# Optimization experiments

Hardware: AMD Instinct MI355X
Metric: run time of the kernel (lower is better)

## Reference

```python
import jax, jax.numpy as jnp
import numpy as np

B = 4096
ED = 128          # EMBEDDING_DIM
HD = 64           # HIDDEN_DIM
LH = 128          # LSTM_HIDDEN_DIM
IN_DIM = ED * (12 + 48 + 1)  # 7808
N_ABILITY, N_MOVE = 300, 900


def setup_inputs() -> dict:
    key = jax.random.key(0)
    ks = jax.random.split(key, 16)
    s = lambda k, shape, scale=0.05: (jax.random.normal(k, shape, dtype=jnp.float32) * scale)
    return {
        "ability_ids": jax.random.randint(ks[0], (B, 12), 0, N_ABILITY),
        "move_ids": jax.random.randint(ks[1], (B, 48), 0, N_MOVE),
        "numerical": s(ks[2], (B, 84), 1.0),
        "mask": (jax.random.uniform(ks[3], (B, 9)) > 0.3).astype(jnp.float32),
        "h0": jnp.zeros((B, LH), jnp.float32),
        "c0": jnp.zeros((B, LH), jnp.float32),
        "ability_emb": s(ks[4], (N_ABILITY, ED), 1.0),
        "move_emb": s(ks[5], (N_MOVE, ED), 1.0),
        "num_W": s(ks[6], (ED, 84)),
        "num_b": s(ks[7], (ED,)),
        "Wih": s(ks[8], (4 * LH, IN_DIM), 0.01),
        "Whh": s(ks[9], (4 * LH, LH)),
        "bih": s(ks[10], (4 * LH,)),
        "bhh": s(ks[11], (4 * LH,)),
        "W1": s(ks[12], (HD, LH)),
        "b1": s(ks[13], (HD,)),
        "W2": s(ks[14], (ED, HD)),
        "b2": s(ks[15], (ED,)),
        "Wa": s(jax.random.fold_in(key, 100), (9, ED)),
        "ba": s(jax.random.fold_in(key, 101), (9,)),
    }


def reference(ability_ids, move_ids, numerical, mask, h0, c0,
              ability_emb, move_emb, num_W, num_b,
              Wih, Whh, bih, bhh, W1, b1, W2, b2, Wa, ba):
    # Gather + concat: [B, 12*ED] + [B, 48*ED] + [B, ED] -> [B, 7808]
    ab = ability_emb[ability_ids].reshape(ability_ids.shape[0], 12 * ED)
    mv = move_emb[move_ids].reshape(move_ids.shape[0], 48 * ED)
    num = numerical @ num_W.T + num_b
    x = jnp.concatenate([ab, mv, num], axis=-1)

    # Single-timestep LSTM (torch gate order: i, f, g, o)
    gates = x @ Wih.T + bih + h0 @ Whh.T + bhh
    i, f, g, o = jnp.split(gates, 4, axis=-1)
    i, f, o = jax.nn.sigmoid(i), jax.nn.sigmoid(f), jax.nn.sigmoid(o)
    g = jnp.tanh(g)
    c1 = f * c0 + i * g
    h1 = o * jnp.tanh(c1)

    # MLP head + action logits
    feat = jax.nn.relu(h1 @ W1.T + b1) @ W2.T + b2
    probs = jax.nn.softmax(feat @ Wa.T + ba, axis=-1)

    # Masked renormalization; fall back to unmasked probs when mask kills everything
    masked = probs * mask
    ssum = masked.sum(-1, keepdims=True)
    out = jnp.where(ssum > 0, masked / jnp.where(ssum > 0, ssum, 1.0), probs)
    return out, h1, c1
```

## Files before the change

kernel.cpp:

```cpp
#include <hip/hip_runtime.h>
#include <hip/hip_bf16.h>
#include <stdint.h>
#include <stddef.h>

typedef __bf16 bf16;
typedef __bf16 bf16x8 __attribute__((ext_vector_type(8)));
typedef float f32x4 __attribute__((ext_vector_type(4)));

#define BATCH 4096
#define KIH 7808
#define KTOT 7936
#define NG 512
#define LH 128
#define HD 64
#define ED 128
#define SPLITK 4

#define OFF_WCAT 0u
#define OFF_GPART 8126464u
#define OFF_XT   41680896u
#define OFF_AB   43778048u
#define OFF_MV   43854848u
#define OFF_ADDR 44085248u
#define OFF_H1B  46182400u
#define OFF_W1F  47230976u
#define OFF_W2F  47247360u
#define OFF_WAF  47263744u

#define O_H1 (BATCH * 9)
#define O_C1 (BATCH * 9 + BATCH * LH)

typedef const __attribute__((address_space(1))) uint32_t* gas_ptr;
typedef __attribute__((address_space(3))) uint32_t* las_ptr;

__device__ __forceinline__ void async16(const void* g, void* l) {
    __builtin_amdgcn_global_load_lds((gas_ptr)g, (las_ptr)l, 16, 0, 0);
}

__global__ void prep(const int* __restrict__ ab_ids,
                     const int* __restrict__ mv_ids,
                     const float* __restrict__ numerical,
                     const float* __restrict__ h0,
                     const float* __restrict__ numW,
                     const float* __restrict__ numb,
                     const float* __restrict__ Wih,
                     const float* __restrict__ Whh,
                     const float* __restrict__ ab_emb,
                     const float* __restrict__ mv_emb,
                     const float* __restrict__ W1,
                     const float* __restrict__ W2,
                     const float* __restrict__ Wa,
                     uint8_t* __restrict__ ws) {
    const int bid = blockIdx.x;
    const int t = threadIdx.x;

    if (bid < BATCH) {
        bf16* xtail = (bf16*)(ws + OFF_XT);
        uint32_t* addrs = (uint32_t*)(ws + OFF_ADDR);
        const int b = bid;

        __shared__ int ids[60];
        __shared__ float numr[84];
        if (t < 60) ids[t] = (t < 12) ? ab_ids[b * 12 + t] : mv_ids[b * 48 + (t - 12)];
        if (t >= 128 && t < 128 + 84) numr[t - 128] = numerical[(size_t)b * 84 + (t - 128)];
        __syncthreads();

        if (t < 128) {
            float acc = numb[t];
#pragma unroll 4
            for (int k = 0; k < 84; ++k)
                acc += numr[k] * numW[t * 84 + k];
            xtail[(size_t)b * 256 + t] = (bf16)acc;
        } else {
            const int tt = t - 128;
            xtail[(size_t)b * 256 + 128 + tt] = (bf16)h0[(size_t)b * LH + tt];
        }

        if (t < 64) {
            uint32_t off;
            if (t < 12) off = OFF_AB + (uint32_t)ids[t] * 256u;
            else if (t < 60) off = OFF_MV + (uint32_t)ids[t] * 256u;
            else if (t == 60) off = OFF_XT + (uint32_t)b * 512u;
            else if (t == 61) off = OFF_XT + (uint32_t)b * 512u + 256u;
            else off = OFF_XT;
            addrs[(size_t)b * 64 + t] = off;
        }
    } else if (bid < BATCH + 512) {
        bf16* Wcat = (bf16*)(ws + OFF_WCAT);
        const int n = bid - BATCH;
        const float* src_ih = Wih + (size_t)n * KIH;
        const float* src_hh = Whh + (size_t)n * LH;
        bf16* dst = Wcat + (size_t)n * KTOT;
        for (int k4 = t; k4 < KTOT / 4; k4 += 256) {
            const int k = k4 * 4;
            const float4 v = (k < KIH) ? *(const float4*)(src_ih + k)
                                       : *(const float4*)(src_hh + (k - KIH));
            bf16 o0 = (bf16)v.x, o1 = (bf16)v.y, o2 = (bf16)v.z, o3 = (bf16)v.w;
            dst[k] = o0; dst[k + 1] = o1; dst[k + 2] = o2; dst[k + 3] = o3;
        }
    } else if (bid < BATCH + 512 + 600) {
        bf16* ab8 = (bf16*)(ws + OFF_AB);
        bf16* mv8 = (bf16*)(ws + OFF_MV);
        const int i = (bid - BATCH - 512) * 256 + t;
        if (i < 300 * 128) ab8[i] = (bf16)ab_emb[i];
        else if (i < 1200 * 128) mv8[i - 300 * 128] = (bf16)mv_emb[i - 300 * 128];
    } else {
        bf16* W1f = (bf16*)(ws + OFF_W1F);
        bf16* W2f = (bf16*)(ws + OFF_W2F);
        bf16* Waf = (bf16*)(ws + OFF_WAF);
        for (int e = t; e < 8192; e += 256) {
            const int j = e & 7, ln = (e >> 3) & 63, fid = e >> 9;
            const int kt = fid & 3, nt = fid >> 2;
            const int n = nt * 16 + (ln & 15);
            const int k = kt * 32 + (ln >> 4) * 8 + j;
            W1f[e] = (bf16)W1[n * 128 + k];
        }
        for (int e = t; e < 8192; e += 256) {
            const int j = e & 7, ln = (e >> 3) & 63, fid = e >> 9;
            const int kt = fid & 1, nt = fid >> 1;
            const int n = nt * 16 + (ln & 15);
            const int k = kt * 32 + (ln >> 4) * 8 + j;
            W2f[e] = (bf16)W2[n * 64 + k];
        }
        for (int e = t; e < 2048; e += 256) {
            const int j = e & 7, ln = (e >> 3) & 63, kt = e >> 9;
            const int n = ln & 15;
            const int k = kt * 32 + (ln >> 4) * 8 + j;
            Waf[e] = (n < 9) ? (bf16)Wa[n * 128 + k] : (bf16)0.f;
        }
    }
}

__global__ __launch_bounds__(256, 2) void gemm_gates(
    const uint8_t* __restrict__ wsbase,
    const bf16* __restrict__ Wcat,
    const uint32_t* __restrict__ addrs,
    float* __restrict__ gpart) {
    __shared__ bf16 As[2][128 * 64];
    __shared__ bf16 Bs[2][128 * 64];
    __shared__ uint32_t adr[17][128];

    const int tid = threadIdx.x;
    const int w = tid >> 6;
    const int lane = tid & 63;
    const int bm = blockIdx.x;
    const int bn = blockIdx.y;
    const int bz = blockIdx.z;
    const int kt_beg = bz * 31;
    const int kt_end = kt_beg + 31;

    const int s0 = kt_beg >> 1;
    const int ns = ((kt_end - 1) >> 1) - s0 + 1;
    for (int i = tid; i < ns * 128; i += 256) {
        adr[i >> 7][i & 127] =
            addrs[(size_t)(bm * 128 + (i & 127)) * 64 + s0 + (i >> 7)];
    }

    const int r_l = lane >> 3;
    const int sc16 = ((lane & 7) ^ r_l) * 16;

    f32x4 acc[4][4];
#pragma unroll
    for (int i = 0; i < 4; ++i)
#pragma unroll
        for (int j = 0; j < 4; ++j)
#pragma unroll
            for (int r = 0; r < 4; ++r) acc[i][j][r] = 0.f;

    const int m0 = (w & 1) * 64;
    const int n0 = (w >> 1) * 64;

    __syncthreads();

    auto stage = [&](int kt, int pb) {
        const int k0 = kt * 64;
        const int sl = (kt >> 1) - s0;
        const int hb = (kt & 1) * 128;
#pragma unroll
        for (int j = 0; j < 4; ++j) {
            const int row = (w * 4 + j) * 8 + r_l;
            const uint8_t* gsrc = wsbase + adr[sl][row] + hb + sc16;
            async16(gsrc, (void*)&As[pb][((w * 4 + j) * 64 + lane) * 8]);
        }
#pragma unroll
        for (int j = 0; j < 4; ++j) {
            const int row = (w * 4 + j) * 8 + r_l;
            const bf16* gsrc = Wcat + (size_t)(bn * 128 + row) * KTOT + k0 + (sc16 >> 1);
            async16(gsrc, (void*)&Bs[pb][((w * 4 + j) * 64 + lane) * 8]);
        }
    };

    stage(kt_beg, 0);

    for (int kt = kt_beg; kt < kt_end; ++kt) {
        const int pb = (kt - kt_beg) & 1;
        __syncthreads();
        if (kt + 1 < kt_end) stage(kt + 1, pb ^ 1);

        const bf16* Ab = &As[pb][0];
        const bf16* Bb = &Bs[pb][0];
#pragma unroll
        for (int ks = 0; ks < 2; ++ks) {
            bf16x8 af[4], bfr[4];
            const int kk8 = ks * 4 + (lane >> 4);
#pragma unroll
            for (int t = 0; t < 4; ++t) {
                const int m = m0 + t * 16 + (lane & 15);
                af[t] = *(const bf16x8*)&Ab[m * 64 + ((kk8 ^ (m & 7)) * 8)];
                const int n = n0 + t * 16 + (lane & 15);
                bfr[t] = *(const bf16x8*)&Bb[n * 64 + ((kk8 ^ (n & 7)) * 8)];
            }
#pragma unroll
            for (int ti = 0; ti < 4; ++ti)
#pragma unroll
                for (int tj = 0; tj < 4; ++tj)
                    acc[ti][tj] = __builtin_amdgcn_mfma_f32_16x16x32_bf16(
                        af[ti], bfr[tj], acc[ti][tj], 0, 0, 0);
        }
    }

    float* gdst = gpart + (size_t)bz * BATCH * NG;
    const int mlo = (lane >> 4) * 4;
    const int nlo = lane & 15;
#pragma unroll
    for (int ti = 0; ti < 4; ++ti)
#pragma unroll
        for (int tj = 0; tj < 4; ++tj) {
            const int mg = bm * 128 + m0 + ti * 16 + mlo;
            const int ng = bn * 128 + n0 + tj * 16 + nlo;
            float* dst = gdst + (size_t)mg * NG + ng;
#pragma unroll
            for (int r = 0; r < 4; ++r)
                dst[(size_t)r * NG] = acc[ti][tj][r];
        }
}

__global__ void reduce_lstm(const float* __restrict__ gpart,
                            const float* __restrict__ bih,
                            const float* __restrict__ bhh,
                            const float* __restrict__ c0,
                            float* __restrict__ out,
                            bf16* __restrict__ h1b) {
    const int t = threadIdx.x;
    const int b = blockIdx.x * 2 + (t >> 7);
    const int u = t & 127;

    float gv[4];
#pragma unroll
    for (int q = 0; q < 4; ++q)
        gv[q] = bih[q * 128 + u] + bhh[q * 128 + u];
#pragma unroll
    for (int z = 0; z < SPLITK; ++z) {
        const float* gz = gpart + ((size_t)z * BATCH + b) * NG + u;
#pragma unroll
        for (int q = 0; q < 4; ++q) gv[q] += gz[q * 128];
    }

    const float iv = 1.f / (1.f + __expf(-gv[0]));
    const float fv = 1.f / (1.f + __expf(-gv[1]));
    const float gg = tanhf(gv[2]);
    const float ov = 1.f / (1.f + __expf(-gv[3]));
    const float c1 = fv * c0[(size_t)b * LH + u] + iv * gg;
    const float h1 = ov * tanhf(c1);

    out[O_H1 + (size_t)b * LH + u] = h1;
    out[O_C1 + (size_t)b * LH + u] = c1;
    h1b[(size_t)b * LH + u] = (bf16)h1;
}

__global__ __launch_bounds__(64) void mlp_head(
    const bf16* __restrict__ h1b, const float* __restrict__ mask,
    const bf16* __restrict__ W1f, const bf16* __restrict__ W2f,
    const bf16* __restrict__ Waf,
    const float* __restrict__ b1, const float* __restrict__ b2,
    const float* __restrict__ ba,
    float* __restrict__ out) {
    __shared__ bf16 uS[16 * 64];
    __shared__ bf16 fS[16 * 128];

    const int lane = threadIdx.x;
    const int b0 = blockIdx.x * 16;
    const int nl = lane & 15, kg = lane >> 4;

    bf16x8 ah[4];
#pragma unroll
    for (int kt = 0; kt < 4; ++kt)
        ah[kt] = *(const bf16x8*)&h1b[(size_t)(b0 + nl) * 128 + kt * 32 + kg * 8];

#pragma unroll
    for (int nt = 0; nt < 4; ++nt) {
        f32x4 a = {0.f, 0.f, 0.f, 0.f};
#pragma unroll
        for (int kt = 0; kt < 4; ++kt)
            a = __builtin_amdgcn_mfma_f32_16x16x32_bf16(
                ah[kt], *(const bf16x8*)&W1f[((nt * 4 + kt) * 64 + lane) * 8],
                a, 0, 0, 0);
        const int n = nt * 16 + nl;
        const float bb = b1[n];
#pragma unroll
        for (int r = 0; r < 4; ++r)
            uS[(kg * 4 + r) * 64 + n] = (bf16)fmaxf(a[r] + bb, 0.f);
    }
    __syncthreads();

    bf16x8 au[2];
#pragma unroll
    for (int kt = 0; kt < 2; ++kt)
        au[kt] = *(const bf16x8*)&uS[nl * 64 + kt * 32 + kg * 8];

#pragma unroll
    for (int nt = 0; nt < 8; ++nt) {
        f32x4 a = {0.f, 0.f, 0.f, 0.f};
#pragma unroll
        for (int kt = 0; kt < 2; ++kt)
            a = __builtin_amdgcn_mfma_f32_16x16x32_bf16(
                au[kt], *(const bf16x8*)&W2f[((nt * 2 + kt) * 64 + lane) * 8],
                a, 0, 0, 0);
        const int n = nt * 16 + nl;
        const float bb = b2[n];
#pragma unroll
        for (int r = 0; r < 4; ++r)
            fS[(kg * 4 + r) * 128 + n] = (bf16)(a[r] + bb);
    }
    __syncthreads();

    bf16x8 afr[4];
#pragma unroll
    for (int kt = 0; kt < 4; ++kt)
        afr[kt] = *(const bf16x8*)&fS[nl * 128 + kt * 32 + kg * 8];

    f32x4 lg4 = {0.f, 0.f, 0.f, 0.f};
#pragma unroll
    for (int kt = 0; kt < 4; ++kt)
        lg4 = __builtin_amdgcn_mfma_f32_16x16x32_bf16(
            afr[kt], *(const bf16x8*)&Waf[(kt * 64 + lane) * 8], lg4, 0, 0, 0);

    const float bav = (nl < 9) ? ba[nl] : 0.f;

#pragma unroll
    for (int r = 0; r < 4; ++r) {
        const int b = b0 + kg * 4 + r;
        float lg = (nl < 9) ? lg4[r] + bav : -1e30f;
        float mx = lg;
#pragma unroll
        for (int off = 1; off < 16; off <<= 1)
            mx = fmaxf(mx, __shfl_xor(mx, off, 64));
        const float e = (nl < 9) ? __expf(lg - mx) : 0.f;
        const float mv = (nl < 9) ? mask[(size_t)b * 9 + nl] : 0.f;
        float tot = e, ms = e * mv;
#pragma unroll
        for (int off = 1; off < 16; off <<= 1) {
            tot += __shfl_xor(tot, off, 64);
            ms += __shfl_xor(ms, off, 64);
        }
        if (nl < 9)
            out[(size_t)b * 9 + nl] = (ms > 0.f) ? e * mv / ms : e / tot;
    }
}

extern "C" void kernel_launch(void* const* d_in, const int* in_sizes, int n_in,
                              void* d_out, int out_size, void* d_ws, size_t ws_size,
                              hipStream_t stream) {
    const int* ab_ids = (const int*)d_in[0];
    const int* mv_ids = (const int*)d_in[1];
    const float* numerical = (const float*)d_in[2];
    const float* mask = (const float*)d_in[3];
    const float* h0 = (const float*)d_in[4];
    const float* c0 = (const float*)d_in[5];
    const float* ab_emb = (const float*)d_in[6];
    const float* mv_emb = (const float*)d_in[7];
    const float* numW = (const float*)d_in[8];
    const float* numb = (const float*)d_in[9];
    const float* Wih = (const float*)d_in[10];
    const float* Whh = (const float*)d_in[11];
    const float* bih = (const float*)d_in[12];
    const float* bhh = (const float*)d_in[13];
    const float* W1 = (const float*)d_in[14];
    const float* b1 = (const float*)d_in[15];
    const float* W2 = (const float*)d_in[16];
    const float* b2 = (const float*)d_in[17];
    const float* Wa = (const float*)d_in[18];
    const float* ba = (const float*)d_in[19];
    float* out = (float*)d_out;

    uint8_t* ws = (uint8_t*)d_ws;
    bf16* Wcat = (bf16*)(ws + OFF_WCAT);
    float* gpart = (float*)(ws + OFF_GPART);
    uint32_t* addrs = (uint32_t*)(ws + OFF_ADDR);
    bf16* h1b = (bf16*)(ws + OFF_H1B);
    bf16* W1f = (bf16*)(ws + OFF_W1F);
    bf16* W2f = (bf16*)(ws + OFF_W2F);
    bf16* Waf = (bf16*)(ws + OFF_WAF);

    prep<<<BATCH + 512 + 600 + 1, 256, 0, stream>>>(
        ab_ids, mv_ids, numerical, h0, numW, numb, Wih, Whh, ab_emb, mv_emb,
        W1, W2, Wa, ws);
    gemm_gates<<<dim3(32, 4, SPLITK), 256, 0, stream>>>(ws, Wcat, addrs, gpart);
    reduce_lstm<<<BATCH / 2, 256, 0, stream>>>(gpart, bih, bhh, c0, out, h1b);
    mlp_head<<<BATCH / 16, 64, 0, stream>>>(h1b, mask, W1f, W2f, Waf,
                                            b1, b2, ba, out);
}
```

Measured before the change: 182.2 us.

## Split GEMM warps along K within block and reduce partials through LDS

Reassigns the four warps from a 2x2 M/N tiling to a 2(N) x 2(K) split, with each warp covering all 128 rows over half of each 64-wide K tile. This means each warp loads only four B fragments per tile and reuses them across eight A fragments. After the main loop, the K-halves are summed through shared memory before the global store. The accumulators double to 128 floats per lane, which raises register pressure and may reduce occupancy. The extra LDS reduction also adds epilogue cost.

```diff
diff --git a/kernel.cpp b/kernel.cpp
--- a/kernel.cpp
+++ b/kernel.cpp
@@ -159,16 +159,19 @@
     const int r_l = lane >> 3;
     const int sc16 = ((lane & 7) ^ r_l) * 16;
 
-    f32x4 acc[4][4];
-#pragma unroll
-    for (int i = 0; i < 4; ++i)
+    const int wn = w & 1;
+    const int wk = w >> 1;
+    const int n0 = wn * 64;
+    const int kk8 = wk * 4 + (lane >> 4);
+    const int fl = lane & 15;
+
+    f32x4 acc[8][4];
+#pragma unroll
+    for (int i = 0; i < 8; ++i)
 #pragma unroll
         for (int j = 0; j < 4; ++j)
 #pragma unroll
             for (int r = 0; r < 4; ++r) acc[i][j][r] = 0.f;
-
-    const int m0 = (w & 1) * 64;
-    const int n0 = (w >> 1) * 64;
 
     __syncthreads();
 
@@ -199,40 +202,53 @@
 
         const bf16* Ab = &As[pb][0];
         const bf16* Bb = &Bs[pb][0];
-#pragma unroll
-        for (int ks = 0; ks < 2; ++ks) {
-            bf16x8 af[4], bfr[4];
-            const int kk8 = ks * 4 + (lane >> 4);
-#pragma unroll
-            for (int t = 0; t < 4; ++t) {
-                const int m = m0 + t * 16 + (lane & 15);
-                af[t] = *(const bf16x8*)&Ab[m * 64 + ((kk8 ^ (m & 7)) * 8)];
-                const int n = n0 + t * 16 + (lane & 15);
-                bfr[t] = *(const bf16x8*)&Bb[n * 64 + ((kk8 ^ (n & 7)) * 8)];
+
+        bf16x8 bfr[4];
+#pragma unroll
+        for (int tj = 0; tj < 4; ++tj) {
+            const int n = n0 + tj * 16 + fl;
+            bfr[tj] = *(const bf16x8*)&Bb[n * 64 + ((kk8 ^ (n & 7)) * 8)];
+        }
+#pragma unroll
+        for (int ti = 0; ti < 8; ++ti) {
+            const int m = ti * 16 + fl;
+            const bf16x8 af = *(const bf16x8*)&Ab[m * 64 + ((kk8 ^ (m & 7)) * 8)];
+#pragma unroll
+            for (int tj = 0; tj < 4; ++tj)
+                acc[ti][tj] = __builtin_amdgcn_mfma_f32_16x16x32_bf16(
+                    af, bfr[tj], acc[ti][tj], 0, 0, 0);
+        }
+    }
+
+    __syncthreads();
+    float* red = (wn == 0) ? (float*)&As[0][0] : (float*)&Bs[0][0];
+    if (wk == 1) {
+#pragma unroll
+        for (int ti = 0; ti < 8; ++ti)
+#pragma unroll
+            for (int tj = 0; tj < 4; ++tj)
+#pragma unroll
+                for (int r = 0; r < 4; ++r)
+                    red[((ti * 4 + tj) * 4 + r) * 64 + lane] = acc[ti][tj][r];
+    }
+    __syncthreads();
+
+    if (wk == 0) {
+        float* gdst = gpart + (size_t)bz * BATCH * NG;
+        const int mlo = (lane >> 4) * 4;
+#pragma unroll
+        for (int ti = 0; ti < 8; ++ti)
+#pragma unroll
+            for (int tj = 0; tj < 4; ++tj) {
+                const int mg = bm * 128 + ti * 16 + mlo;
+                const int ng = bn * 128 + n0 + tj * 16 + fl;
+                float* dst = gdst + (size_t)mg * NG + ng;
+#pragma unroll
+                for (int r = 0; r < 4; ++r)
+                    dst[(size_t)r * NG] =
+                        acc[ti][tj][r] + red[((ti * 4 + tj) * 4 + r) * 64 + lane];
             }
-#pragma unroll
-            for (int ti = 0; ti < 4; ++ti)
-#pragma unroll
-                for (int tj = 0; tj < 4; ++tj)
-                    acc[ti][tj] = __builtin_amdgcn_mfma_f32_16x16x32_bf16(
-                        af[ti], bfr[tj], acc[ti][tj], 0, 0, 0);
-        }
-    }
-
-    float* gdst = gpart + (size_t)bz * BATCH * NG;
-    const int mlo = (lane >> 4) * 4;
-    const int nlo = lane & 15;
-#pragma unroll
-    for (int ti = 0; ti < 4; ++ti)
-#pragma unroll
-        for (int tj = 0; tj < 4; ++tj) {
-            const int mg = bm * 128 + m0 + ti * 16 + mlo;
-            const int ng = bn * 128 + n0 + tj * 16 + nlo;
-            float* dst = gdst + (size_t)mg * NG + ng;
-#pragma unroll
-            for (int r = 0; r < 4; ++r)
-                dst[(size_t)r * NG] = acc[ti][tj][r];
-        }
+    }
 }
 
 __global__ void reduce_lstm(const float* __restrict__ gpart,
```

Measured after the change: 181.0 us. About the same (-0.7%).
